# Kernel optimization log

Hardware: AMD Instinct MI355X
Metric: run time of the kernel (lower is better)

The kernel has to match this reference:

```python
import jax, jax.numpy as jnp
import numpy as np
from jax import lax
from jax.scipy.special import logsumexp

B, L, H, T = 64, 512, 768, 16


def setup_inputs() -> dict:
    key = jax.random.key(0)
    ks = jax.random.split(key, 6)
    return {
        "hidden_state": jax.random.normal(ks[0], (B, L, H), dtype=jnp.float32),
        "attention_mask": jnp.ones((B, L), dtype=jnp.int32),
        "labels": jax.random.randint(ks[1], (B, L), 0, T),
        "classifier_w": jax.random.normal(ks[2], (T, H), dtype=jnp.float32) * 0.02,
        "classifier_b": jnp.zeros((T,), dtype=jnp.float32),
        "start_trans": jax.random.normal(ks[3], (T,), dtype=jnp.float32) * 0.1,
        "end_trans": jax.random.normal(ks[4], (T,), dtype=jnp.float32) * 0.1,
        "trans": jax.random.normal(ks[5], (T,), dtype=jnp.float32)[:, None] * 0.0
                 + jax.random.normal(ks[5], (T, T), dtype=jnp.float32) * 0.1,
    }


def _crf_numerator(emissions, labels, mask, start_trans, end_trans, trans):
    # emissions [B,L,T], labels [B,L], mask [B,L] float
    em = jnp.take_along_axis(emissions, labels[..., None], axis=-1)[..., 0]  # [B,L]
    tr = trans[labels[:, :-1], labels[:, 1:]]                                # [B,L-1]
    score = start_trans[labels[:, 0]] + em[:, 0]
    score = score + jnp.sum(mask[:, 1:] * (tr + em[:, 1:]), axis=1)
    seq_ends = jnp.sum(mask, axis=1).astype(jnp.int32) - 1                   # [B]
    last_tags = jnp.take_along_axis(labels, seq_ends[:, None], axis=1)[:, 0]
    return score + end_trans[last_tags]


def _crf_denominator(emissions, mask, start_trans, end_trans, trans):
    # forward algorithm with masking; scan over time
    init = start_trans[None, :] + emissions[:, 0]  # [B,T]

    def step(score, xs):
        m, em = xs  # m [B], em [B,T]
        nxt = logsumexp(score[:, :, None] + trans[None] + em[:, None, :], axis=1)
        score = jnp.where(m[:, None] > 0, nxt, score)
        return score, None

    xs = (jnp.swapaxes(mask[:, 1:], 0, 1), jnp.swapaxes(emissions[:, 1:], 0, 1))
    final, _ = lax.scan(step, init, xs)
    return logsumexp(final + end_trans[None, :], axis=1)  # [B]


def _viterbi_single(emissions, start_trans, end_trans, trans):
    # emissions [L,T]; decode without mask (as in the torch code: self.crf.decode(logits))
    score0 = start_trans + emissions[0]

    def step(score, em):
        nxt = score[:, None] + trans + em[None, :]  # [T,T]
        return jnp.max(nxt, axis=0), jnp.argmax(nxt, axis=0)

    final, history = lax.scan(step, score0, emissions[1:])  # history [L-1,T]
    last = jnp.argmax(final + end_trans)

    def back(tag, hist):
        prev = hist[tag]
        return prev, prev

    _, tags_rev = lax.scan(back, last, history, reverse=True)
    return jnp.concatenate([tags_rev, last[None]])  # [L]


def reference(hidden_state, attention_mask, labels, classifier_w, classifier_b,
              start_trans, end_trans, trans):
    # dropout is identity at inference/reference time
    logits = jnp.einsum("blh,th->blt", hidden_state, classifier_w) + classifier_b  # [B,L,T]
    maskf = attention_mask.astype(logits.dtype)
    numer = _crf_numerator(logits, labels, maskf, start_trans, end_trans, trans)
    denom = _crf_denominator(logits, maskf, start_trans, end_trans, trans)
    llh = numer - denom
    loss = -jnp.mean(llh)  # reduction='mean' over batch
    tags = jax.vmap(_viterbi_single, in_axes=(0, None, None, None))(
        logits, start_trans, end_trans, trans)  # [B,L] int
    return loss, tags.astype(jnp.float32)
```

## Files before the change

kernel.cpp:

```cpp
#include <hip/hip_runtime.h>
#include <cstdint>

#define Bn 64
#define Ln 512
#define Hn 768
#define Tn 16
#define Cn 8
#define Sn 64
#define Kn 4
#define Kc 192
#define Mrows (Bn*Ln)
#define LOG16 2.7725887222397812f

__global__ __launch_bounds__(256, 4) void k_gemm_part(
    const float* __restrict__ hs, const float* __restrict__ W,
    float* __restrict__ partial, float* __restrict__ lossws) {
  int bx = blockIdx.x;
  int tid = threadIdx.x;
  if (bx == 0 && tid == 0) {
    lossws[0] = 0.f;
    ((int*)lossws)[1] = 0;
  }
  int rt = bx >> 2, s = bx & 3;
  int r0 = rt * 128, kb = s * Kc;
  int row = (tid & 63) + ((tid >> 7) << 6);
  int t0 = ((tid >> 6) & 1) * 8;
  __shared__ float alds[128 * 36];
  __shared__ float wlds[16 * 192];
  float acc[8] = {0.f};
  for (int idx = tid; idx < 768; idx += 256) {
    int t = idx / 48, jj = idx - t * 48;
    *(float4*)&wlds[t * 192 + jj * 4] = *(const float4*)(W + (size_t)t * Hn + kb + jj * 4);
  }
  int rr = tid >> 3, jj4 = (tid & 7) * 4;
  const float* s0 = hs + (size_t)(r0 + rr)      * Hn + kb + jj4;
  const float* s1 = hs + (size_t)(r0 + rr + 32) * Hn + kb + jj4;
  const float* s2 = hs + (size_t)(r0 + rr + 64) * Hn + kb + jj4;
  const float* s3 = hs + (size_t)(r0 + rr + 96) * Hn + kb + jj4;
  float* d0 = &alds[(rr)      * 36 + jj4];
  float* d1 = &alds[(rr + 32) * 36 + jj4];
  float* d2 = &alds[(rr + 64) * 36 + jj4];
  float* d3 = &alds[(rr + 96) * 36 + jj4];
  float4 pv0 = *(const float4*)(s0);
  float4 pv1 = *(const float4*)(s1);
  float4 pv2 = *(const float4*)(s2);
  float4 pv3 = *(const float4*)(s3);
#pragma unroll 1
  for (int cc = 0; cc < 6; ++cc) {
    *(float4*)d0 = pv0;
    *(float4*)d1 = pv1;
    *(float4*)d2 = pv2;
    *(float4*)d3 = pv3;
    __syncthreads();
    if (cc < 5) {
      int off = (cc + 1) * 32;
      pv0 = *(const float4*)(s0 + off);
      pv1 = *(const float4*)(s1 + off);
      pv2 = *(const float4*)(s2 + off);
      pv3 = *(const float4*)(s3 + off);
    }
#pragma unroll
    for (int j = 0; j < 8; ++j) {
      float4 a = *(const float4*)&alds[row * 36 + j * 4];
#pragma unroll
      for (int tt = 0; tt < 8; ++tt) {
        float4 wv = *(const float4*)&wlds[(t0 + tt) * 192 + cc * 32 + j * 4];
        acc[tt] = fmaf(a.x, wv.x, fmaf(a.y, wv.y, fmaf(a.z, wv.z, fmaf(a.w, wv.w, acc[tt]))));
      }
    }
    __syncthreads();
  }
  float* dst = partial + ((size_t)s * Mrows + (r0 + row)) * Tn + t0;
  *(float4*)(dst + 0) = make_float4(acc[0], acc[1], acc[2], acc[3]);
  *(float4*)(dst + 4) = make_float4(acc[4], acc[5], acc[6], acc[7]);
}

__global__ __launch_bounds__(256) void k_em_scan(
    const float* __restrict__ partial, const float* __restrict__ bias,
    const int* __restrict__ mask, const float* __restrict__ trans,
    float* __restrict__ em, float* __restrict__ qmat,
    float* __restrict__ qv, uint8_t* __restrict__ hist) {
  int half = blockIdx.x >> 9, bc = blockIdx.x & 511;
  int b = bc >> 3, c = bc & 7;
  int tid = threadIdx.x, i = tid >> 4, tp = tid & 15;
  int l0 = c * Sn;
  __shared__ float ems[Sn * Tn];
  __shared__ int msk[Sn];
  __shared__ float pbuf[256];
  __shared__ uint8_t hl[Tn * Sn * Tn];
#pragma unroll
  for (int g = 0; g < 4; ++g) {
    int rl = (tid >> 4) + g * 16, t = tid & 15;
    int grow = bc * Sn + rl;
    float sum = bias[t];
#pragma unroll
    for (int s = 0; s < Kn; ++s) sum += partial[((size_t)s * Mrows + grow) * Tn + t];
    float mx = sum;
    mx = fmaxf(mx, __shfl_xor(mx, 1));
    mx = fmaxf(mx, __shfl_xor(mx, 2));
    mx = fmaxf(mx, __shfl_xor(mx, 4));
    mx = fmaxf(mx, __shfl_xor(mx, 8));
    float ev = sum - (mx + LOG16);
    ems[rl * Tn + t] = ev;
    if (half == 0) em[(size_t)grow * Tn + t] = ev;
  }
  if (tid < Sn) msk[tid] = mask[b * Ln + l0 + tid];
  __syncthreads();
  int lstart = (c == 0) ? 1 : l0;
  int gb = i << 4;
  if (half == 0) {
    float etr[Tn];
#pragma unroll
    for (int t = 0; t < Tn; ++t) etr[t] = __expf(trans[t * Tn + tp]);
    float p = (tp == i) ? 1.f : 0.f;
    float logs = 0.f;
    for (int l = lstart; l < l0 + Sn; ++l) {
      pbuf[tid] = p;
      __builtin_amdgcn_sched_barrier(0);
      float4 q0 = *(const float4*)&pbuf[gb + 0];
      float4 q1 = *(const float4*)&pbuf[gb + 4];
      float4 q2 = *(const float4*)&pbuf[gb + 8];
      float4 q3 = *(const float4*)&pbuf[gb + 12];
      float cs = __expf(ems[(l - l0) * Tn + tp]);
      float dot = 0.f;
      dot = fmaf(q0.x, etr[0],  dot); dot = fmaf(q0.y, etr[1],  dot);
      dot = fmaf(q0.z, etr[2],  dot); dot = fmaf(q0.w, etr[3],  dot);
      dot = fmaf(q1.x, etr[4],  dot); dot = fmaf(q1.y, etr[5],  dot);
      dot = fmaf(q1.z, etr[6],  dot); dot = fmaf(q1.w, etr[7],  dot);
      dot = fmaf(q2.x, etr[8],  dot); dot = fmaf(q2.y, etr[9],  dot);
      dot = fmaf(q2.z, etr[10], dot); dot = fmaf(q2.w, etr[11], dot);
      dot = fmaf(q3.x, etr[12], dot); dot = fmaf(q3.y, etr[13], dot);
      dot = fmaf(q3.z, etr[14], dot); dot = fmaf(q3.w, etr[15], dot);
      float pn = dot * cs;
      p = msk[l - l0] ? pn : p;
      if ((l & 15) == 15) {
        float m = p;
        m = fmaxf(m, __shfl_xor(m, 1));
        m = fmaxf(m, __shfl_xor(m, 2));
        m = fmaxf(m, __shfl_xor(m, 4));
        m = fmaxf(m, __shfl_xor(m, 8));
        p /= m;
        logs += __logf(m);
      }
    }
    qmat[(((size_t)b * Cn + c) * Tn + i) * Tn + tp] = __logf(p) + logs;
  } else {
    float tcol[Tn];
#pragma unroll
    for (int t = 0; t < Tn; ++t) tcol[t] = trans[t * Tn + tp];
    float v = (tp == i) ? 0.f : -1e30f;
    for (int l = lstart; l < l0 + Sn; ++l) {
      pbuf[tid] = v;
      __builtin_amdgcn_sched_barrier(0);
      float4 q0 = *(const float4*)&pbuf[gb + 0];
      float4 q1 = *(const float4*)&pbuf[gb + 4];
      float4 q2 = *(const float4*)&pbuf[gb + 8];
      float4 q3 = *(const float4*)&pbuf[gb + 12];
      float best = -3.0e38f; int arg = 0;
#define VSTEP(val, t) { float cand = (val) + tcol[t]; bool g = cand > best; \
                        arg = g ? (t) : arg; best = g ? cand : best; }
      VSTEP(q0.x, 0)  VSTEP(q0.y, 1)  VSTEP(q0.z, 2)  VSTEP(q0.w, 3)
      VSTEP(q1.x, 4)  VSTEP(q1.y, 5)  VSTEP(q1.z, 6)  VSTEP(q1.w, 7)
      VSTEP(q2.x, 8)  VSTEP(q2.y, 9)  VSTEP(q2.z, 10) VSTEP(q2.w, 11)
      VSTEP(q3.x, 12) VSTEP(q3.y, 13) VSTEP(q3.z, 14) VSTEP(q3.w, 15)
#undef VSTEP
      v = best + ems[(l - l0) * Tn + tp];
      hl[(i * Sn + (l - l0)) * Tn + tp] = (uint8_t)arg;
    }
    qv[(((size_t)b * Cn + c) * Tn + i) * Tn + tp] = v;
    __syncthreads();
    const uint4* s4 = (const uint4*)hl;
    uint4* d4 = (uint4*)(hist + (size_t)bc * (Tn * Sn * Tn));
    for (int k = tid; k < (Tn * Sn * Tn) / 16; k += 256) d4[k] = s4[k];
  }
}

__global__ __launch_bounds__(512) void k_tail(
    const float* __restrict__ qv, const float* __restrict__ em,
    const float* __restrict__ start, const float* __restrict__ endt,
    const uint8_t* __restrict__ hist, const int* __restrict__ labels,
    const int* __restrict__ mask, const float* __restrict__ trans,
    const float* __restrict__ qmat, float* __restrict__ lossws,
    float* __restrict__ loss_out, float* __restrict__ tags) {
  int bid = blockIdx.x, tid = threadIdx.x;
  __shared__ float qs[Cn * Tn * Tn];
  if (bid >= Bn) {
    int b = bid - Bn;
    {
      float4 qv4 = *(((const float4*)qmat) + (size_t)b * 512 + tid);
      *(((float4*)qs) + tid) = qv4;
    }
    {
      int l = tid;
      int y = labels[b * Ln + l];
      int m = mask[b * Ln + l];
      float s;
      if (l == 0) s = start[y] + em[((size_t)b * Ln) * Tn + y];
      else s = m ? (trans[labels[b * Ln + l - 1] * Tn + y] + em[((size_t)b * Ln + l) * Tn + y]) : 0.f;
      int msum = m;
      for (int off = 32; off; off >>= 1) {
        s += __shfl_down(s, off);
        msum += __shfl_down(msum, off);
      }
      __shared__ float sw[8]; __shared__ int mw[8];
      __shared__ float snum;
      int wid = tid >> 6, ln = tid & 63;
      if (ln == 0) { sw[wid] = s; mw[wid] = msum; }
      __syncthreads();
      if (tid == 0) {
        float st = 0.f; int mt = 0;
        for (int wv = 0; wv < 8; ++wv) { st += sw[wv]; mt += mw[wv]; }
        snum = st + endt[labels[b * Ln + mt - 1]];
      }
      __syncthreads();
      if (tid < Tn) {
        int k = tid;
        float p = start[k] + em[((size_t)b * Ln) * Tn + k];
        for (int c = 0; c < Cn; ++c) {
          float vals[Tn]; float mx = -3.0e38f;
#pragma unroll
          for (int i2 = 0; i2 < Tn; ++i2) {
            float cand = __shfl(p, i2, 16) + qs[c * 256 + i2 * 16 + k];
            vals[i2] = cand;
            mx = fmaxf(mx, cand);
          }
          float sm = 0.f;
#pragma unroll
          for (int i2 = 0; i2 < Tn; ++i2) sm += __expf(vals[i2] - mx);
          p = mx + __logf(sm);
        }
        float x = p + endt[k];
        float mx = x;
        mx = fmaxf(mx, __shfl_xor(mx, 1));
        mx = fmaxf(mx, __shfl_xor(mx, 2));
        mx = fmaxf(mx, __shfl_xor(mx, 4));
        mx = fmaxf(mx, __shfl_xor(mx, 8));
        float e = __expf(x - mx);
        e += __shfl_xor(e, 1);
        e += __shfl_xor(e, 2);
        e += __shfl_xor(e, 4);
        e += __shfl_xor(e, 8);
        float denom = mx + __logf(e);
        if (k == 0) {
          atomicAdd(&lossws[0], snum - denom);
          __threadfence();
          int ticket = atomicAdd((int*)lossws + 1, 1);
          if (ticket == Bn - 1) {
            __threadfence();
            float total = atomicAdd(&lossws[0], 0.f);
            loss_out[0] = -total * (1.0f / Bn);
          }
        }
      }
    }
    return;
  }
  int b = bid;
  __shared__ int Bs[Cn][Tn];
  __shared__ int bnd[Cn + 1];
  {
    float4 qv4 = *(((const float4*)qv) + (size_t)b * 512 + tid);
    *(((float4*)qs) + tid) = qv4;
  }
  __syncthreads();
  if (tid < Tn) {
    int k = tid;
    float p = start[k] + em[((size_t)b * Ln) * Tn + k];
    for (int c = 0; c < Cn; ++c) {
      float best = -3.0e38f; int arg = 0;
#pragma unroll
      for (int i2 = 0; i2 < Tn; ++i2) {
        float cand = __shfl(p, i2, 16) + qs[c * 256 + i2 * 16 + k];
        bool g = cand > best;
        arg = g ? i2 : arg;
        best = g ? cand : best;
      }
      Bs[c][k] = arg;
      p = best;
    }
    float x = p + endt[k]; int idx = k;
#pragma unroll
    for (int d = 1; d < 16; d <<= 1) {
      float xo = __shfl_xor(x, d);
      int io = __shfl_xor(idx, d);
      bool take = (xo > x) || (xo == x && io < idx);
      x = take ? xo : x;
      idx = take ? io : idx;
    }
    if (k == 0) bnd[Cn] = idx;
  }
  __syncthreads();
  if (tid == 0) {
    int t = bnd[Cn];
    for (int c = Cn - 1; c >= 0; --c) { t = Bs[c][t]; bnd[c] = t; }
  }
  __syncthreads();
  int w = tid >> 6, lane = tid & 63;
  int istar = bnd[w];
  int cur = bnd[w + 1];
  int l0 = w * Sn;
  const uint4* hp = (const uint4*)(hist + ((size_t)(b * Cn + w) * Tn + istar) * (Sn * Tn));
  uint4 hh = hp[lane];
  float mytag = (lane == 63) ? (float)cur : 0.f;
  for (int l = l0 + 63; l >= l0 + 1; --l) {
    int sl = l - l0;
    unsigned w0 = __shfl((int)hh.x, sl);
    unsigned w1 = __shfl((int)hh.y, sl);
    unsigned w2 = __shfl((int)hh.z, sl);
    unsigned w3 = __shfl((int)hh.w, sl);
    unsigned word = (cur < 8) ? ((cur < 4) ? w0 : w1) : ((cur < 12) ? w2 : w3);
    cur = (int)((word >> ((cur & 3) * 8)) & 0xff);
    if (lane == sl - 1) mytag = (float)cur;
  }
  tags[(size_t)b * Ln + l0 + lane] = mytag;
}

extern "C" void kernel_launch(void* const* d_in, const int* in_sizes, int n_in,
                              void* d_out, int out_size, void* d_ws, size_t ws_size,
                              hipStream_t stream) {
  const float* hs     = (const float*)d_in[0];
  const int*   mask   = (const int*)d_in[1];
  const int*   labels = (const int*)d_in[2];
  const float* W      = (const float*)d_in[3];
  const float* bias   = (const float*)d_in[4];
  const float* start  = (const float*)d_in[5];
  const float* endt   = (const float*)d_in[6];
  const float* trans  = (const float*)d_in[7];
  float* out = (float*)d_out;

  char* ws = (char*)d_ws;
  float*   em      = (float*)(ws);
  float*   qmat    = (float*)(ws + 2097152);
  float*   qv      = (float*)(ws + 2621440);
  float*   lossws  = (float*)(ws + 3145728);
  float*   partial = (float*)(ws + 3149824);
  uint8_t* hist    = (uint8_t*)(ws + 11538432);

  hipLaunchKernelGGL(k_gemm_part, dim3(1024), dim3(256), 0, stream, hs, W, partial, lossws);
  hipLaunchKernelGGL(k_em_scan,   dim3(1024), dim3(256), 0, stream, partial, bias, mask, trans, em, qmat, qv, hist);
  hipLaunchKernelGGL(k_tail,      dim3(128),  dim3(512), 0, stream, qv, em, start, endt, hist, labels, mask, trans, qmat, lossws, out, out + 1);
}
```

Measured before the change: 204.9 us.

## Shorten CRF scan dependency chains with tree reductions and retile GEMM output

The GEMM partial kernel now assigns each wave 4 tags over two 64-row halves instead of 8 tags over one row. Its output is staged through LDS so global stores are fully coalesced float4 writes. In the forward and Viterbi scans, the serial 16-term FMA chain and compare chain become balanced pairwise trees, cutting per-step latency on the sequential recurrence. The exp of emissions is precomputed into shared memory so it is off the scan loop. Tree argmax breaks ties toward the lower index, matching the original strict greater-than order, and the sum order changes only float rounding.

```diff
diff --git a/kernel.cpp b/kernel.cpp
--- a/kernel.cpp
+++ b/kernel.cpp
@@ -23,11 +23,13 @@
   }
   int rt = bx >> 2, s = bx & 3;
   int r0 = rt * 128, kb = s * Kc;
-  int row = (tid & 63) + ((tid >> 7) << 6);
-  int t0 = ((tid >> 6) & 1) * 8;
+  int lane = tid & 63, wid = tid >> 6;
+  int row_a = lane;
+  int t0 = wid * 4;
   __shared__ float alds[128 * 36];
   __shared__ float wlds[16 * 192];
-  float acc[8] = {0.f};
+  float accA0 = 0.f, accA1 = 0.f, accA2 = 0.f, accA3 = 0.f;
+  float accB0 = 0.f, accB1 = 0.f, accB2 = 0.f, accB3 = 0.f;
   for (int idx = tid; idx < 768; idx += 256) {
     int t = idx / 48, jj = idx - t * 48;
     *(float4*)&wlds[t * 192 + jj * 4] = *(const float4*)(W + (size_t)t * Hn + kb + jj * 4);
@@ -61,18 +63,45 @@
     }
 #pragma unroll
     for (int j = 0; j < 8; ++j) {
-      float4 a = *(const float4*)&alds[row * 36 + j * 4];
-#pragma unroll
-      for (int tt = 0; tt < 8; ++tt) {
-        float4 wv = *(const float4*)&wlds[(t0 + tt) * 192 + cc * 32 + j * 4];
-        acc[tt] = fmaf(a.x, wv.x, fmaf(a.y, wv.y, fmaf(a.z, wv.z, fmaf(a.w, wv.w, acc[tt]))));
-      }
+      float4 aa = *(const float4*)&alds[row_a * 36 + j * 4];
+      float4 ab = *(const float4*)&alds[(row_a + 64) * 36 + j * 4];
+      float4 w0 = *(const float4*)&wlds[(t0 + 0) * 192 + cc * 32 + j * 4];
+      float4 w1 = *(const float4*)&wlds[(t0 + 1) * 192 + cc * 32 + j * 4];
+      float4 w2 = *(const float4*)&wlds[(t0 + 2) * 192 + cc * 32 + j * 4];
+      float4 w3 = *(const float4*)&wlds[(t0 + 3) * 192 + cc * 32 + j * 4];
+      accA0 = fmaf(aa.x, w0.x, fmaf(aa.y, w0.y, fmaf(aa.z, w0.z, fmaf(aa.w, w0.w, accA0))));
+      accA1 = fmaf(aa.x, w1.x, fmaf(aa.y, w1.y, fmaf(aa.z, w1.z, fmaf(aa.w, w1.w, accA1))));
+      accA2 = fmaf(aa.x, w2.x, fmaf(aa.y, w2.y, fmaf(aa.z, w2.z, fmaf(aa.w, w2.w, accA2))));
+      accA3 = fmaf(aa.x, w3.x, fmaf(aa.y, w3.y, fmaf(aa.z, w3.z, fmaf(aa.w, w3.w, accA3))));
+      accB0 = fmaf(ab.x, w0.x, fmaf(ab.y, w0.y, fmaf(ab.z, w0.z, fmaf(ab.w, w0.w, accB0))));
+      accB1 = fmaf(ab.x, w1.x, fmaf(ab.y, w1.y, fmaf(ab.z, w1.z, fmaf(ab.w, w1.w, accB1))));
+      accB2 = fmaf(ab.x, w2.x, fmaf(ab.y, w2.y, fmaf(ab.z, w2.z, fmaf(ab.w, w2.w, accB2))));
+      accB3 = fmaf(ab.x, w3.x, fmaf(ab.y, w3.y, fmaf(ab.z, w3.z, fmaf(ab.w, w3.w, accB3))));
     }
     __syncthreads();
   }
-  float* dst = partial + ((size_t)s * Mrows + (r0 + row)) * Tn + t0;
-  *(float4*)(dst + 0) = make_float4(acc[0], acc[1], acc[2], acc[3]);
-  *(float4*)(dst + 4) = make_float4(acc[4], acc[5], acc[6], acc[7]);
+  float* outs = alds;
+  outs[row_a * 17 + t0 + 0] = accA0;
+  outs[row_a * 17 + t0 + 1] = accA1;
+  outs[row_a * 17 + t0 + 2] = accA2;
+  outs[row_a * 17 + t0 + 3] = accA3;
+  outs[(row_a + 64) * 17 + t0 + 0] = accB0;
+  outs[(row_a + 64) * 17 + t0 + 1] = accB1;
+  outs[(row_a + 64) * 17 + t0 + 2] = accB2;
+  outs[(row_a + 64) * 17 + t0 + 3] = accB3;
+  __syncthreads();
+  float* base = partial + ((size_t)s * Mrows + r0) * Tn;
+  int v1 = tid, v2 = tid + 256;
+  float4 o1 = make_float4(outs[(v1 >> 2) * 17 + (v1 & 3) * 4 + 0],
+                          outs[(v1 >> 2) * 17 + (v1 & 3) * 4 + 1],
+                          outs[(v1 >> 2) * 17 + (v1 & 3) * 4 + 2],
+                          outs[(v1 >> 2) * 17 + (v1 & 3) * 4 + 3]);
+  float4 o2 = make_float4(outs[(v2 >> 2) * 17 + (v2 & 3) * 4 + 0],
+                          outs[(v2 >> 2) * 17 + (v2 & 3) * 4 + 1],
+                          outs[(v2 >> 2) * 17 + (v2 & 3) * 4 + 2],
+                          outs[(v2 >> 2) * 17 + (v2 & 3) * 4 + 3]);
+  *(float4*)(base + v1 * 4) = o1;
+  *(float4*)(base + v2 * 4) = o2;
 }
 
 __global__ __launch_bounds__(256) void k_em_scan(
@@ -85,6 +114,7 @@
   int tid = threadIdx.x, i = tid >> 4, tp = tid & 15;
   int l0 = c * Sn;
   __shared__ float ems[Sn * Tn];
+  __shared__ float cse[Sn * Tn];
   __shared__ int msk[Sn];
   __shared__ float pbuf[256];
   __shared__ uint8_t hl[Tn * Sn * Tn];
@@ -102,6 +132,7 @@
     mx = fmaxf(mx, __shfl_xor(mx, 8));
     float ev = sum - (mx + LOG16);
     ems[rl * Tn + t] = ev;
+    cse[rl * Tn + t] = __expf(ev);
     if (half == 0) em[(size_t)grow * Tn + t] = ev;
   }
   if (tid < Sn) msk[tid] = mask[b * Ln + l0 + tid];
@@ -121,17 +152,13 @@
       float4 q1 = *(const float4*)&pbuf[gb + 4];
       float4 q2 = *(const float4*)&pbuf[gb + 8];
       float4 q3 = *(const float4*)&pbuf[gb + 12];
-      float cs = __expf(ems[(l - l0) * Tn + tp]);
-      float dot = 0.f;
-      dot = fmaf(q0.x, etr[0],  dot); dot = fmaf(q0.y, etr[1],  dot);
-      dot = fmaf(q0.z, etr[2],  dot); dot = fmaf(q0.w, etr[3],  dot);
-      dot = fmaf(q1.x, etr[4],  dot); dot = fmaf(q1.y, etr[5],  dot);
-      dot = fmaf(q1.z, etr[6],  dot); dot = fmaf(q1.w, etr[7],  dot);
-      dot = fmaf(q2.x, etr[8],  dot); dot = fmaf(q2.y, etr[9],  dot);
-      dot = fmaf(q2.z, etr[10], dot); dot = fmaf(q2.w, etr[11], dot);
-      dot = fmaf(q3.x, etr[12], dot); dot = fmaf(q3.y, etr[13], dot);
-      dot = fmaf(q3.z, etr[14], dot); dot = fmaf(q3.w, etr[15], dot);
-      float pn = dot * cs;
+      float a0  = q0.x * etr[0],  a1  = q0.y * etr[1],  a2  = q0.z * etr[2],  a3  = q0.w * etr[3];
+      float a4  = q1.x * etr[4],  a5  = q1.y * etr[5],  a6  = q1.z * etr[6],  a7  = q1.w * etr[7];
+      float a8  = q2.x * etr[8],  a9  = q2.y * etr[9],  a10 = q2.z * etr[10], a11 = q2.w * etr[11];
+      float a12 = q3.x * etr[12], a13 = q3.y * etr[13], a14 = q3.z * etr[14], a15 = q3.w * etr[15];
+      float dot = (((a0 + a1) + (a2 + a3)) + ((a4 + a5) + (a6 + a7)))
+                + (((a8 + a9) + (a10 + a11)) + ((a12 + a13) + (a14 + a15)));
+      float pn = dot * cse[(l - l0) * Tn + tp];
       p = msk[l - l0] ? pn : p;
       if ((l & 15) == 15) {
         float m = p;
@@ -156,14 +183,27 @@
       float4 q1 = *(const float4*)&pbuf[gb + 4];
       float4 q2 = *(const float4*)&pbuf[gb + 8];
       float4 q3 = *(const float4*)&pbuf[gb + 12];
-      float best = -3.0e38f; int arg = 0;
-#define VSTEP(val, t) { float cand = (val) + tcol[t]; bool g = cand > best; \
-                        arg = g ? (t) : arg; best = g ? cand : best; }
-      VSTEP(q0.x, 0)  VSTEP(q0.y, 1)  VSTEP(q0.z, 2)  VSTEP(q0.w, 3)
-      VSTEP(q1.x, 4)  VSTEP(q1.y, 5)  VSTEP(q1.z, 6)  VSTEP(q1.w, 7)
-      VSTEP(q2.x, 8)  VSTEP(q2.y, 9)  VSTEP(q2.z, 10) VSTEP(q2.w, 11)
-      VSTEP(q3.x, 12) VSTEP(q3.y, 13) VSTEP(q3.z, 14) VSTEP(q3.w, 15)
-#undef VSTEP
+      float c0  = q0.x + tcol[0],  c1  = q0.y + tcol[1],  c2  = q0.z + tcol[2],  c3  = q0.w + tcol[3];
+      float c4  = q1.x + tcol[4],  c5  = q1.y + tcol[5],  c6  = q1.z + tcol[6],  c7  = q1.w + tcol[7];
+      float c8  = q2.x + tcol[8],  c9  = q2.y + tcol[9],  c10 = q2.z + tcol[10], c11 = q2.w + tcol[11];
+      float c12 = q3.x + tcol[12], c13 = q3.y + tcol[13], c14 = q3.z + tcol[14], c15 = q3.w + tcol[15];
+      bool g; float v01,v23,v45,v67,v89,vAB,vCD,vEF,v03,v47,v8B,vCF,v07,v8F,best;
+      int i01,i23,i45,i67,i89,iAB,iCD,iEF,i03,i47,i8B,iCF,i07,i8F,arg;
+      g = c1  > c0;  v01 = g ? c1  : c0;  i01 = g ? 1  : 0;
+      g = c3  > c2;  v23 = g ? c3  : c2;  i23 = g ? 3  : 2;
+      g = c5  > c4;  v45 = g ? c5  : c4;  i45 = g ? 5  : 4;
+      g = c7  > c6;  v67 = g ? c7  : c6;  i67 = g ? 7  : 6;
+      g = c9  > c8;  v89 = g ? c9  : c8;  i89 = g ? 9  : 8;
+      g = c11 > c10; vAB = g ? c11 : c10; iAB = g ? 11 : 10;
+      g = c13 > c12; vCD = g ? c13 : c12; iCD = g ? 13 : 12;
+      g = c15 > c14; vEF = g ? c15 : c14; iEF = g ? 15 : 14;
+      g = v23 > v01; v03 = g ? v23 : v01; i03 = g ? i23 : i01;
+      g = v67 > v45; v47 = g ? v67 : v45; i47 = g ? i67 : i45;
+      g = vAB > v89; v8B = g ? vAB : v89; i8B = g ? iAB : i89;
+      g = vEF > vCD; vCF = g ? vEF : vCD; iCF = g ? iEF : iCD;
+      g = v47 > v03; v07 = g ? v47 : v03; i07 = g ? i47 : i03;
+      g = vCF > v8B; v8F = g ? vCF : v8B; i8F = g ? iCF : i8B;
+      g = v8F > v07; best = g ? v8F : v07; arg = g ? i8F : i07;
       v = best + ems[(l - l0) * Tn + tp];
       hl[(i * Sn + (l - l0)) * Tn + tp] = (uint8_t)arg;
     }
```

Result: no change. 205.6 us (+0.4%).
